# Performance work log

Measured on AMD Instinct MI355X. Metric: run time of the kernel, lower is better.

Reference implementation:

```python
import jax, jax.numpy as jnp
import numpy as np

BOX = 256      # box_size
OS = 1         # oversampling
NC = 10        # n_classes
B = 16         # batch
N = 262144     # points per example


def setup_inputs() -> dict:
    key = jax.random.key(0)
    k1, k2 = jax.random.split(key)
    # coordinates in [-0.5, 0.5) so (points+0.5)*S lies inside the grid
    points = jax.random.uniform(k1, (B, 2, N), dtype=jnp.float32, minval=-0.5, maxval=0.5)
    values = jax.random.normal(k2, (B, NC, N), dtype=jnp.float32)
    return {"points": points, "values": values}


def reference(points, values):
    S = BOX * OS
    b, nc = points.shape[0], values.shape[1]
    # [B,2,N] -> [B,N,2], scaled into pixel coords
    p = jnp.swapaxes((points + 0.5) * S, 1, 2)
    xyf = jnp.floor(p)
    r = p - xyf                       # fractional part, [B,N,2]
    xy = xyf.astype(jnp.int32)
    x, y = xy[..., 0], xy[..., 1]     # [B,N]
    rx, ry = r[..., 0], r[..., 1]

    im = jnp.zeros((b, nc, S * S), dtype=values.dtype)

    def scat(acc, idx, contrib):
        # acc [NC, S*S], idx [N], contrib [NC, N]
        return acc.at[:, idx].add(contrib)

    scat_b = jax.vmap(scat)  # over batch

    # 4-corner bilinear (CIC) deposition
    for dx in (0, 1):
        x_ = x + dx
        wx = (1 - dx) + (2 * dx - 1) * rx
        for dy in (0, 1):
            y_ = y + dy
            wy = (1 - dy) + (2 * dy - 1) * ry
            valid = (x_ >= 0) & (x_ < S) & (y_ >= 0) & (y_ < S)
            idx = jnp.where(valid, y_ * S + x_, 0)           # [B,N]
            w = jnp.where(valid, wx * wy, 0.0)               # [B,N]
            im = scat_b(im, idx, w[:, None, :] * values)     # [B,NC,S*S]

    return im.reshape(b, nc, S, S)
```

## Files before the change

### kernel.cpp

```cpp
#include <hip/hip_runtime.h>

#define S_     256
#define NC_    10
#define CHUNK  2048
#define NBIN   256
#define CAP    1536
#define RSTR   7

typedef unsigned int u32;

__device__ __forceinline__ u32 f2bf(float f) {
    u32 u = __float_as_uint(f);
    return (u + 0x7fffu + ((u >> 16) & 1u)) >> 16;
}
__device__ __forceinline__ float bf2f(u32 h) { return __uint_as_float(h << 16); }


__global__ void __launch_bounds__(256)
k_hist(const float* __restrict__ points, u32* __restrict__ hist, int N) {
    __shared__ u32 h[NBIN];
    h[threadIdx.x] = 0;
    __syncthreads();
    const int cpb = N / CHUNK;
    const int b  = blockIdx.x / cpb;
    const int n0 = (blockIdx.x % cpb) * CHUNK;
    const float* pb = points + (size_t)b * 2 * N;
    for (int i = threadIdx.x; i < CHUNK; i += 256) {
        int n = n0 + i;
        float px = (pb[n] + 0.5f) * (float)S_;
        float py = (pb[(size_t)N + n] + 0.5f) * (float)S_;
        int xi = (int)floorf(px), yi = (int)floorf(py);
        int bin = ((yi >> 4) << 4) + (xi >> 4);
        atomicAdd(&h[bin], 1u);
    }
    __syncthreads();
    hist[(size_t)blockIdx.x * NBIN + threadIdx.x] = h[threadIdx.x];
}

__global__ void __launch_bounds__(256)
k_scan(const u32* __restrict__ hist, u32* __restrict__ blockStart,
       u32* __restrict__ binBase, u32* __restrict__ binCnt, int cpb, int N) {
    __shared__ u32 s[256];
    const int b = blockIdx.x, t = threadIdx.x;
    u32 tot = 0;
    for (int i = 0; i < cpb; ++i) tot += hist[(size_t)(b * cpb + i) * NBIN + t];
    s[t] = tot;
    __syncthreads();
    for (int off = 1; off < 256; off <<= 1) {
        u32 y = (t >= off) ? s[t - off] : 0;
        __syncthreads();
        s[t] += y;
        __syncthreads();
    }
    u32 base = (u32)b * (u32)N + s[t] - tot;
    binBase[b * NBIN + t] = base;
    binCnt[b * NBIN + t]  = tot;
    u32 run = base;
    for (int i = 0; i < cpb; ++i) {
        size_t idx = (size_t)(b * cpb + i) * NBIN + t;
        u32 hv = hist[idx];
        blockStart[idx] = run;
        run += hv;
    }
}

__global__ void __launch_bounds__(256)
k_scatter(const float* __restrict__ points, const float* __restrict__ values,
          const u32* __restrict__ blockStart, uint2* __restrict__ recs, int N) {
    __shared__ u32 cnt[NBIN];
    __shared__ u32 sc[NBIN];
    __shared__ u32 gOff[NBIN];
    __shared__ u32 recDst[CHUNK];
    __shared__ uint2 lrec[CHUNK * 3];

    const int tid = threadIdx.x;
    const int cpb = N / CHUNK;
    const int b  = blockIdx.x / cpb;
    const int n0 = (blockIdx.x % cpb) * CHUNK;
    const float* pb = points + (size_t)b * 2 * N;
    const float* vb = values + (size_t)b * NC_ * N;

    cnt[tid] = 0;
    __syncthreads();

    const int PPT = CHUNK / 256;
    u32 w0[PPT];
    u32 binArr[PPT];
#pragma unroll
    for (int k = 0; k < PPT; ++k) {
        int n = n0 + tid + k * 256;
        float px = (pb[n] + 0.5f) * (float)S_;
        float py = (pb[(size_t)N + n] + 0.5f) * (float)S_;
        int xi = (int)floorf(px), yi = (int)floorf(py);
        u32 qx = __float2uint_rn((px - (float)(xi & ~15)) * 2048.0f);
        u32 qy = __float2uint_rn((py - (float)(yi & ~15)) * 2048.0f);
        qx = min(qx, 32767u); qy = min(qy, 32767u);
        w0[k] = qx | (qy << 16);
        binArr[k] = (u32)(((yi >> 4) << 4) + (xi >> 4));
        atomicAdd(&cnt[binArr[k]], 1u);
    }
    __syncthreads();

    u32 c = cnt[tid];
    sc[tid] = c;
    __syncthreads();
    for (int off = 1; off < 256; off <<= 1) {
        u32 y = (tid >= off) ? sc[tid - off] : 0;
        __syncthreads();
        sc[tid] += y;
        __syncthreads();
    }
    u32 excl = sc[tid] - c;
    gOff[tid] = blockStart[(size_t)blockIdx.x * NBIN + tid] - excl;
    __syncthreads();
    cnt[tid] = excl;
    __syncthreads();

#pragma unroll
    for (int k = 0; k < PPT; ++k) {
        int n = n0 + tid + k * 256;
        float v[NC_];
#pragma unroll
        for (int cc = 0; cc < NC_; ++cc) v[cc] = vb[(size_t)cc * N + n];
        u32 bin = binArr[k];
        u32 slot = atomicAdd(&cnt[bin], 1u);
        recDst[slot] = gOff[bin] + slot;
        lrec[slot * 3]     = make_uint2(w0[k],
                                        f2bf(v[0]) | (f2bf(v[1]) << 16));
        lrec[slot * 3 + 1] = make_uint2(f2bf(v[2]) | (f2bf(v[3]) << 16),
                                        f2bf(v[4]) | (f2bf(v[5]) << 16));
        lrec[slot * 3 + 2] = make_uint2(f2bf(v[6]) | (f2bf(v[7]) << 16),
                                        f2bf(v[8]) | (f2bf(v[9]) << 16));
    }
    __syncthreads();

    for (int p = tid; p < CHUNK * 3; p += 256) {
        u32 r = (u32)p / 3u;
        u32 cidx = (u32)p - r * 3u;
        recs[(size_t)recDst[r] * 3u + cidx] = lrec[p];
    }
}

__global__ void __launch_bounds__(256)
k_fused(const uint2* __restrict__ recs, const u32* __restrict__ binBase,
        const u32* __restrict__ binCnt, float* __restrict__ out,
        float* __restrict__ borderBuf) {
    __shared__ u32 cnt[NBIN];
    __shared__ u32 excl[NBIN];
    __shared__ u32 sc[NBIN];
    __shared__ u32 lrec[CAP * RSTR];

    const int tid = threadIdx.x;
    const int g = blockIdx.x;
    const int batch = g >> 8, t = g & 255;
    const int ox = (t & 15) * 16, oy = (t >> 4) * 16;
    const u32 base = binBase[g];
    const u32 n = min(binCnt[g], (u32)CAP);

    cnt[tid] = 0;
    __syncthreads();

    u32 r[6][6];
    int cell[6];
#pragma unroll
    for (int k = 0; k < 6; ++k) {
        int i = k * 256 + tid;
        cell[k] = -1;
        if (i < (int)n) {
            size_t sa = (size_t)(base + i) * 3;
            uint2 a = recs[sa], b2 = recs[sa + 1], c2 = recs[sa + 2];
            r[k][0] = a.x;  r[k][1] = a.y;
            r[k][2] = b2.x; r[k][3] = b2.y;
            r[k][4] = c2.x; r[k][5] = c2.y;
            u32 qx = a.x & 0xffffu, qy = a.x >> 16;
            cell[k] = (int)(((qy >> 11) << 4) | (qx >> 11));
            atomicAdd(&cnt[cell[k]], 1u);
        }
    }
    __syncthreads();

    u32 c = cnt[tid];
    sc[tid] = c;
    __syncthreads();
    for (int off = 1; off < 256; off <<= 1) {
        u32 y = (tid >= off) ? sc[tid - off] : 0;
        __syncthreads();
        sc[tid] += y;
        __syncthreads();
    }
    excl[tid] = sc[tid] - c;
    __syncthreads();
    cnt[tid] = excl[tid];
    __syncthreads();

#pragma unroll
    for (int k = 0; k < 6; ++k) {
        if (cell[k] >= 0) {
            u32 o = atomicAdd(&cnt[cell[k]], 1u) * RSTR;
#pragma unroll
            for (int w = 0; w < 6; ++w) lrec[o + w] = r[k][w];
        }
    }
    __syncthreads();

    for (int p = tid; p < 289; p += 256) {
        int lx = p % 17, ly = p / 17;
        float acc[NC_];
#pragma unroll
        for (int q = 0; q < NC_; ++q) acc[q] = 0.0f;
#pragma unroll
        for (int dy = 0; dy < 2; ++dy) {
            int cy = ly - 1 + dy;
            if ((unsigned)cy >= 16u) continue;
#pragma unroll
            for (int dx = 0; dx < 2; ++dx) {
                int cx = lx - 1 + dx;
                if ((unsigned)cx >= 16u) continue;
                int cc = (cy << 4) | cx;
                u32 j1 = cnt[cc];
                for (u32 j = excl[cc]; j < j1; ++j) {
                    u32 o = j * RSTR;
                    u32 w0 = lrec[o];
                    float rx = (float)(w0 & 2047u)         * (1.0f / 2048.0f);
                    float ry = (float)((w0 >> 16) & 2047u) * (1.0f / 2048.0f);
                    float w = (dx ? (1.0f - rx) : rx) * (dy ? (1.0f - ry) : ry);
                    u32 w1 = lrec[o + 1], w2 = lrec[o + 2], w3 = lrec[o + 3],
                        w4 = lrec[o + 4], w5 = lrec[o + 5];
                    acc[0] += w * bf2f(w1 & 0xffffu); acc[1] += w * bf2f(w1 >> 16);
                    acc[2] += w * bf2f(w2 & 0xffffu); acc[3] += w * bf2f(w2 >> 16);
                    acc[4] += w * bf2f(w3 & 0xffffu); acc[5] += w * bf2f(w3 >> 16);
                    acc[6] += w * bf2f(w4 & 0xffffu); acc[7] += w * bf2f(w4 >> 16);
                    acc[8] += w * bf2f(w5 & 0xffffu); acc[9] += w * bf2f(w5 >> 16);
                }
            }
        }
        bool interior = (lx >= 1) & (lx <= 15) & (ly >= 1) & (ly <= 15);
        if (interior) {
            int gx = ox + lx, gy = oy + ly;
            float* ob = out + (size_t)batch * NC_ * S_ * S_ + gy * S_ + gx;
#pragma unroll
            for (int q = 0; q < NC_; ++q) ob[(size_t)q * S_ * S_] = acc[q];
        } else {
            float* bb = borderBuf + ((size_t)g * 289 + p) * NC_;
#pragma unroll
            for (int q = 0; q < NC_; ++q) bb[q] = acc[q];
        }
    }
}

__global__ void __launch_bounds__(256)
k_border(const float* __restrict__ borderBuf, float* __restrict__ out) {
    int idx = blockIdx.x * 256 + threadIdx.x;
    int b = idx >> 16, rem = idx & 65535;
    int gy = rem >> 8, gx = rem & 255;
    bool bx = (gx & 15) == 0, by = (gy & 15) == 0;
    if (!bx && !by) return;

    int txs[2], lxs[2], nx = 0;
    if (bx) {
        if (gx > 0) { txs[nx] = (gx >> 4) - 1; lxs[nx] = 16; ++nx; }
        txs[nx] = gx >> 4; lxs[nx] = 0; ++nx;
    } else { txs[0] = gx >> 4; lxs[0] = gx & 15; nx = 1; }
    int tys[2], lys[2], ny = 0;
    if (by) {
        if (gy > 0) { tys[ny] = (gy >> 4) - 1; lys[ny] = 16; ++ny; }
        tys[ny] = gy >> 4; lys[ny] = 0; ++ny;
    } else { tys[0] = gy >> 4; lys[0] = gy & 15; ny = 1; }

    float acc[NC_];
#pragma unroll
    for (int q = 0; q < NC_; ++q) acc[q] = 0.0f;
    for (int j = 0; j < ny; ++j)
        for (int i = 0; i < nx; ++i) {
            int g = (b << 8) + (tys[j] << 4) + txs[i];
            int p = lys[j] * 17 + lxs[i];
            const float* bb = borderBuf + ((size_t)g * 289 + p) * NC_;
#pragma unroll
            for (int q = 0; q < NC_; ++q) acc[q] += bb[q];
        }
    float* ob = out + (size_t)b * NC_ * S_ * S_ + gy * S_ + gx;
#pragma unroll
    for (int q = 0; q < NC_; ++q) ob[(size_t)q * S_ * S_] = acc[q];
}

__global__ void __launch_bounds__(256)
k_cleanup(const uint2* __restrict__ recs, const u32* __restrict__ binBase,
          const u32* __restrict__ binCnt, float* __restrict__ out, int nTiles) {
    int g = blockIdx.x * 256 + threadIdx.x;
    if (g >= nTiles) return;
    u32 n = binCnt[g];
    if (n <= (u32)CAP) return;
    int batch = g >> 8, t = g & 255;
    int ox = (t & 15) * 16, oy = (t >> 4) * 16;
    u32 base = binBase[g];
    float* ob = out + (size_t)batch * NC_ * S_ * S_;
    for (u32 i = CAP; i < n; ++i) {
        size_t sa = (size_t)(base + i) * 3;
        uint2 a = recs[sa], b2 = recs[sa + 1], c2 = recs[sa + 2];
        u32 qx = a.x & 0xffffu, qy = a.x >> 16;
        int xi = ox + (int)(qx >> 11), yi = oy + (int)(qy >> 11);
        float rx = (float)(qx & 2047u) * (1.0f / 2048.0f);
        float ry = (float)(qy & 2047u) * (1.0f / 2048.0f);
        float v[NC_];
        v[0] = bf2f(a.y & 0xffffu);  v[1] = bf2f(a.y >> 16);
        v[2] = bf2f(b2.x & 0xffffu); v[3] = bf2f(b2.x >> 16);
        v[4] = bf2f(b2.y & 0xffffu); v[5] = bf2f(b2.y >> 16);
        v[6] = bf2f(c2.x & 0xffffu); v[7] = bf2f(c2.x >> 16);
        v[8] = bf2f(c2.y & 0xffffu); v[9] = bf2f(c2.y >> 16);
        for (int dx = 0; dx < 2; ++dx) {
            int x_ = xi + dx; if (x_ >= S_) continue;
            float wx = dx ? rx : (1.0f - rx);
            for (int dy = 0; dy < 2; ++dy) {
                int y_ = yi + dy; if (y_ >= S_) continue;
                float w = wx * (dy ? ry : (1.0f - ry));
                for (int c = 0; c < NC_; ++c)
                    atomicAdd(ob + (size_t)c * S_ * S_ + y_ * S_ + x_, w * v[c]);
            }
        }
    }
}

__global__ void __launch_bounds__(256)
scatter_cic_kernel(const float* __restrict__ points,
                   const float* __restrict__ values,
                   float* __restrict__ out, int N) {
    const int n = blockIdx.x * blockDim.x + threadIdx.x;
    const int b = blockIdx.y;
    if (n >= N) return;
    const float* pb = points + (size_t)b * 2 * N;
    const float px = (pb[n] + 0.5f) * (float)S_;
    const float py = (pb[(size_t)N + n] + 0.5f) * (float)S_;
    const float xf = floorf(px), yf = floorf(py);
    const float rx = px - xf, ry = py - yf;
    const int xi = (int)xf, yi = (int)yf;
    const float* vb = values + (size_t)b * NC_ * N + n;
    float v[NC_];
#pragma unroll
    for (int c = 0; c < NC_; ++c) v[c] = vb[(size_t)c * N];
    float* ob = out + (size_t)b * NC_ * S_ * S_;
#pragma unroll
    for (int dx = 0; dx < 2; ++dx) {
        const int x_ = xi + dx;
        if (x_ < 0 || x_ >= S_) continue;
        const float wx = dx ? rx : (1.0f - rx);
#pragma unroll
        for (int dy = 0; dy < 2; ++dy) {
            const int y_ = yi + dy;
            if (y_ < 0 || y_ >= S_) continue;
            const float w = wx * (dy ? ry : (1.0f - ry));
            const int idx = y_ * S_ + x_;
#pragma unroll
            for (int c = 0; c < NC_; ++c)
                atomicAdd(ob + (size_t)c * S_ * S_ + idx, w * v[c]);
        }
    }
}

extern "C" void kernel_launch(void* const* d_in, const int* in_sizes, int n_in,
                              void* d_out, int out_size, void* d_ws, size_t ws_size,
                              hipStream_t stream) {
    const float* points = (const float*)d_in[0];
    const float* values = (const float*)d_in[1];
    float* out = (float*)d_out;

    const int B = out_size / (NC_ * S_ * S_);
    const int N = in_sizes[0] / (2 * B);

    const size_t P = (size_t)B * N;
    const int cpb = N / CHUNK;
    const int chunksTotal = B * cpb;
    const int nTiles = B * NBIN;

    const size_t recBytes    = P * 24;
    const size_t histElems   = (size_t)chunksTotal * NBIN;
    const size_t borderElems = (size_t)nTiles * 289 * NC_;
    const size_t wsNeeded    = recBytes + 2 * histElems * 4 +
                               2 * (size_t)nTiles * 4 + borderElems * 4 + 256;

    const bool fast = (N % CHUNK == 0) && (N >= CHUNK) && (B > 0) &&
                      (P < (1u << 31) / 2) && (ws_size >= wsNeeded);

    if (fast) {
        char* w = (char*)d_ws;
        uint2* recsA     = (uint2*)w;
        u32* hist        = (u32*)(w + recBytes);
        u32* blockStart  = hist + histElems;
        u32* binBase     = blockStart + histElems;
        u32* binCnt      = binBase + nTiles;
        float* borderBuf = (float*)(binCnt + nTiles);

        k_hist<<<chunksTotal, 256, 0, stream>>>(points, hist, N);
        k_scan<<<B, 256, 0, stream>>>(hist, blockStart, binBase, binCnt, cpb, N);
        k_scatter<<<chunksTotal, 256, 0, stream>>>(points, values, blockStart, recsA, N);
        k_fused<<<nTiles, 256, 0, stream>>>(recsA, binBase, binCnt, out, borderBuf);
        k_border<<<(B * 65536) / 256, 256, 0, stream>>>(borderBuf, out);
        k_cleanup<<<(nTiles + 255) / 256, 256, 0, stream>>>(recsA, binBase, binCnt, out, nTiles);
    } else {
        hipMemsetAsync(d_out, 0, (size_t)out_size * sizeof(float), stream);
        dim3 block(256, 1, 1);
        dim3 grid((N + 255) / 256, B, 1);
        scatter_cic_kernel<<<grid, block, 0, stream>>>(points, values, out, N);
    }
}
```

Baseline: 422.4 us.

## Halve scatter chunk, shrink scatter LDS, and launch border kernel only on seam pixels

Halves the scatter/hist chunk size and replaces the per-record destination array and interleaved record staging in shared memory with a byte bin id plus six structure-of-arrays word planes. Destinations are recomputed at write-out from the bin offset. Shared memory per scatter block drops, which should allow more blocks per CU, though there are now twice as many chunks for the scan to walk. The border kernel's grid now covers only the seam pixels (7936 per batch) instead of every pixel with early exit, and unroll pragmas are added to the scan loops.

```diff
diff --git a/kernel.cpp b/kernel.cpp
--- a/kernel.cpp
+++ b/kernel.cpp
@@ -2,7 +2,7 @@
 
 #define S_     256
 #define NC_    10
-#define CHUNK  2048
+#define CHUNK  1024
 #define NBIN   256
 #define CAP    1536
 #define RSTR   7
@@ -43,6 +43,7 @@
     __shared__ u32 s[256];
     const int b = blockIdx.x, t = threadIdx.x;
     u32 tot = 0;
+#pragma unroll 8
     for (int i = 0; i < cpb; ++i) tot += hist[(size_t)(b * cpb + i) * NBIN + t];
     s[t] = tot;
     __syncthreads();
@@ -56,6 +57,7 @@
     binBase[b * NBIN + t] = base;
     binCnt[b * NBIN + t]  = tot;
     u32 run = base;
+#pragma unroll 4
     for (int i = 0; i < cpb; ++i) {
         size_t idx = (size_t)(b * cpb + i) * NBIN + t;
         u32 hv = hist[idx];
@@ -70,8 +72,8 @@
     __shared__ u32 cnt[NBIN];
     __shared__ u32 sc[NBIN];
     __shared__ u32 gOff[NBIN];
-    __shared__ u32 recDst[CHUNK];
-    __shared__ uint2 lrec[CHUNK * 3];
+    __shared__ unsigned char binId[CHUNK];
+    __shared__ u32 lw[6][CHUNK];
 
     const int tid = threadIdx.x;
     const int cpb = N / CHUNK;
@@ -124,20 +126,22 @@
         for (int cc = 0; cc < NC_; ++cc) v[cc] = vb[(size_t)cc * N + n];
         u32 bin = binArr[k];
         u32 slot = atomicAdd(&cnt[bin], 1u);
-        recDst[slot] = gOff[bin] + slot;
-        lrec[slot * 3]     = make_uint2(w0[k],
-                                        f2bf(v[0]) | (f2bf(v[1]) << 16));
-        lrec[slot * 3 + 1] = make_uint2(f2bf(v[2]) | (f2bf(v[3]) << 16),
-                                        f2bf(v[4]) | (f2bf(v[5]) << 16));
-        lrec[slot * 3 + 2] = make_uint2(f2bf(v[6]) | (f2bf(v[7]) << 16),
-                                        f2bf(v[8]) | (f2bf(v[9]) << 16));
+        binId[slot] = (unsigned char)bin;
+        lw[0][slot] = w0[k];
+        lw[1][slot] = f2bf(v[0]) | (f2bf(v[1]) << 16);
+        lw[2][slot] = f2bf(v[2]) | (f2bf(v[3]) << 16);
+        lw[3][slot] = f2bf(v[4]) | (f2bf(v[5]) << 16);
+        lw[4][slot] = f2bf(v[6]) | (f2bf(v[7]) << 16);
+        lw[5][slot] = f2bf(v[8]) | (f2bf(v[9]) << 16);
     }
     __syncthreads();
 
     for (int p = tid; p < CHUNK * 3; p += 256) {
         u32 r = (u32)p / 3u;
         u32 cidx = (u32)p - r * 3u;
-        recs[(size_t)recDst[r] * 3u + cidx] = lrec[p];
+        u32 dst = gOff[binId[r]] + r;
+        recs[(size_t)dst * 3u + cidx] = make_uint2(lw[2 * cidx][r],
+                                                   lw[2 * cidx + 1][r]);
     }
 }
 
@@ -249,14 +253,24 @@
 }
 
 __global__ void __launch_bounds__(256)
-k_border(const float* __restrict__ borderBuf, float* __restrict__ out) {
+k_border(const float* __restrict__ borderBuf, float* __restrict__ out, int total) {
     int idx = blockIdx.x * 256 + threadIdx.x;
-    int b = idx >> 16, rem = idx & 65535;
-    int gy = rem >> 8, gx = rem & 255;
+    if (idx >= total) return;
+    int b = idx / 7936;
+    int j = idx - b * 7936;
+    int gx, gy;
+    if (j < 4096) {
+        gx = (j >> 8) << 4;
+        gy = j & 255;
+    } else {
+        int j2 = j - 4096;
+        int row = j2 / 240, col = j2 - row * 240;
+        gy = row << 4;
+        gx = col + 1 + col / 15;
+    }
+
+    int txs[2], lxs[2], nx = 0;
     bool bx = (gx & 15) == 0, by = (gy & 15) == 0;
-    if (!bx && !by) return;
-
-    int txs[2], lxs[2], nx = 0;
     if (bx) {
         if (gx > 0) { txs[nx] = (gx >> 4) - 1; lxs[nx] = 16; ++nx; }
         txs[nx] = gx >> 4; lxs[nx] = 0; ++nx;
@@ -270,10 +284,10 @@
     float acc[NC_];
 #pragma unroll
     for (int q = 0; q < NC_; ++q) acc[q] = 0.0f;
-    for (int j = 0; j < ny; ++j)
-        for (int i = 0; i < nx; ++i) {
-            int g = (b << 8) + (tys[j] << 4) + txs[i];
-            int p = lys[j] * 17 + lxs[i];
+    for (int jj = 0; jj < ny; ++jj)
+        for (int ii = 0; ii < nx; ++ii) {
+            int g = (b << 8) + (tys[jj] << 4) + txs[ii];
+            int p = lys[jj] * 17 + lxs[ii];
             const float* bb = borderBuf + ((size_t)g * 289 + p) * NC_;
 #pragma unroll
             for (int q = 0; q < NC_; ++q) acc[q] += bb[q];
@@ -393,7 +407,8 @@
         k_scan<<<B, 256, 0, stream>>>(hist, blockStart, binBase, binCnt, cpb, N);
         k_scatter<<<chunksTotal, 256, 0, stream>>>(points, values, blockStart, recsA, N);
         k_fused<<<nTiles, 256, 0, stream>>>(recsA, binBase, binCnt, out, borderBuf);
-        k_border<<<(B * 65536) / 256, 256, 0, stream>>>(borderBuf, out);
+        const int borderTotal = B * 7936;
+        k_border<<<(borderTotal + 255) / 256, 256, 0, stream>>>(borderBuf, out, borderTotal);
         k_cleanup<<<(nTiles + 255) / 256, 256, 0, stream>>>(recsA, binBase, binCnt, out, nTiles);
     } else {
         hipMemsetAsync(d_out, 0, (size_t)out_size * sizeof(float), stream);
```

Result: no change. 415.8 us (-1.6%).
